# Kernel optimization log

Hardware: AMD Instinct MI355X
Metric: run time of the kernel (lower is better)

## Reference

```python
import jax, jax.numpy as jnp
from jax import lax
import numpy as np

B, T, D_IN = 4, 1024, 8
D_MODEL, N_LAYERS, HORIZON, D_OUT = 512, 2, 24, 8
D_STATE, D_CONV, EXPAND = 64, 4, 2
D_INNER = EXPAND * D_MODEL
DT_RANK = -(-D_MODEL // 16)  # ceil(d_model/16) = 32
LN_EPS = 1e-5


def setup_inputs() -> dict:
    key = jax.random.key(0)
    ks = iter(jax.random.split(key, 24))
    rn = lambda shape, s: jax.random.normal(next(ks), shape, jnp.float32) * s
    A_log = jnp.tile(jnp.log(jnp.arange(1, D_STATE + 1, dtype=jnp.float32)), (N_LAYERS, D_INNER, 1))
    return {
        "x": rn((B, T, D_IN), 1.0),
        "W_in": rn((D_IN, D_MODEL), 0.3), "b_in": jnp.zeros((D_MODEL,), jnp.float32),
        "W_xz": rn((N_LAYERS, D_MODEL, 2 * D_INNER), 0.04),
        "conv_w": rn((N_LAYERS, D_INNER, D_CONV), 0.3), "conv_b": jnp.zeros((N_LAYERS, D_INNER), jnp.float32),
        "W_xproj": rn((N_LAYERS, D_INNER, DT_RANK + 2 * D_STATE), 0.03),
        "W_dt": rn((N_LAYERS, DT_RANK, D_INNER), 0.1), "b_dt": rn((N_LAYERS, D_INNER), 0.1) - 4.0,
        "A_log": A_log, "D_skip": jnp.ones((N_LAYERS, D_INNER), jnp.float32),
        "W_out": rn((N_LAYERS, D_INNER, D_MODEL), 0.03),
        "ln_g": jnp.ones((D_MODEL,), jnp.float32), "ln_b": jnp.zeros((D_MODEL,), jnp.float32),
        "W_h1": rn((D_MODEL, D_MODEL), 0.04), "b_h1": jnp.zeros((D_MODEL,), jnp.float32),
        "W_h2": rn((D_MODEL, HORIZON * D_OUT), 0.04), "b_h2": jnp.zeros((HORIZON * D_OUT,), jnp.float32),
    }


def mamba_block(h, Wxz, cw, cb, Wxp, Wdt, bdt, Alog, Dsk, Wout):
    # h: [B,T,d_model] -> [B,T,d_model]  (mamba-ssm Mamba block, no residual)
    xz = h @ Wxz                                   # [B,T,2*d_inner]
    xb, z = jnp.split(xz, 2, axis=-1)
    # depthwise causal conv over time
    xc = jnp.transpose(xb, (0, 2, 1))              # [B,d_inner,T]
    xc = lax.conv_general_dilated(xc, cw[:, None, :], (1,), [(D_CONV - 1, 0)],
                                  feature_group_count=D_INNER)
    xc = jax.nn.silu(xc + cb[None, :, None])
    xc = jnp.transpose(xc, (0, 2, 1))              # [B,T,d_inner]
    # input-dependent dt, B, C
    xdb = xc @ Wxp                                 # [B,T,dt_rank+2*d_state]
    dt_r = xdb[..., :DT_RANK]
    Bc = xdb[..., DT_RANK:DT_RANK + D_STATE]
    Cc = xdb[..., DT_RANK + D_STATE:]
    dt = jax.nn.softplus(dt_r @ Wdt + bdt)         # [B,T,d_inner]
    A = -jnp.exp(Alog)                             # [d_inner,d_state]

    def step(hst, ins):
        dt_t, B_t, C_t, x_t = ins                  # [B,d_inner],[B,N],[B,N],[B,d_inner]
        dA = jnp.exp(dt_t[..., None] * A)          # [B,d_inner,N]
        hst = dA * hst + dt_t[..., None] * B_t[:, None, :] * x_t[..., None]
        y = jnp.einsum('bdn,bn->bd', hst, C_t)
        return hst, y

    h0 = jnp.zeros((h.shape[0], D_INNER, D_STATE), h.dtype)
    xs = (jnp.transpose(dt, (1, 0, 2)), jnp.transpose(Bc, (1, 0, 2)),
          jnp.transpose(Cc, (1, 0, 2)), jnp.transpose(xc, (1, 0, 2)))
    _, ys = lax.scan(step, h0, xs)                 # ys: [T,B,d_inner]
    y = jnp.transpose(ys, (1, 0, 2)) + Dsk * xc
    y = y * jax.nn.silu(z)
    return y @ Wout


def reference(x, W_in, b_in, W_xz, conv_w, conv_b, W_xproj, W_dt, b_dt, A_log, D_skip,
              W_out, ln_g, ln_b, W_h1, b_h1, W_h2, b_h2):
    h = x @ W_in + b_in                            # [B,T,d_model]
    for i in range(N_LAYERS):
        h = mamba_block(h, W_xz[i], conv_w[i], conv_b[i], W_xproj[i], W_dt[i],
                        b_dt[i], A_log[i], D_skip[i], W_out[i])
    mu = jnp.mean(h, axis=-1, keepdims=True)
    var = jnp.mean(jnp.square(h - mu), axis=-1, keepdims=True)
    h = (h - mu) * lax.rsqrt(var + LN_EPS) * ln_g + ln_b
    last = h[:, -1, :]                             # [B,d_model]
    hid = jax.nn.gelu(last @ W_h1 + b_h1, approximate=False)
    yhat = hid @ W_h2 + b_h2                       # [B,horizon*d_out]
    return yhat.reshape(x.shape[0], HORIZON, D_OUT)
```

## Files before the change

### kernel.cpp

```cpp
#include <hip/hip_runtime.h>
#include <hip/hip_bf16.h>

static constexpr int kB      = 4;
static constexpr int kT      = 1024;
static constexpr int kDIN    = 8;
static constexpr int kDMODEL = 512;
static constexpr int kNLAYER = 2;
static constexpr int kHOR    = 24;
static constexpr int kDOUT   = 8;
static constexpr int kDSTATE = 64;
static constexpr int kDINNER = 1024;
static constexpr int kDTRANK = 32;
static constexpr int kXPROJ  = 160;
static constexpr int kXPAD   = 256;
static constexpr int kBT     = kB * kT;

typedef __bf16 bf16x8 __attribute__((ext_vector_type(8)));
typedef float  f32x4  __attribute__((ext_vector_type(4)));

__device__ __forceinline__ float silu_f(float x)     { return x / (1.f + __expf(-x)); }
__device__ __forceinline__ float softplus_f(float x) { return (x > 20.f) ? x : log1pf(__expf(x)); }
__device__ __forceinline__ float gelu_f(float x)     { return 0.5f * x * (1.f + erff(x * 0.70710678118654752f)); }

__device__ __forceinline__ void gld_lds16(const void* g, void* l) {
    __builtin_amdgcn_global_load_lds(
        (const __attribute__((address_space(1))) unsigned int*)g,
        (__attribute__((address_space(3))) unsigned int*)l, 16, 0, 0);
}

__global__ __launch_bounds__(256) void wtrans_kernel(
    const float* __restrict__ in, int K, int N, int in_lstride,
    __hip_bfloat16* __restrict__ out, int Kpad, int out_lstride)
{
    __shared__ float tile[32][33];
    const int tid = threadIdx.x;
    const int n0 = blockIdx.x * 32;
    const int k0 = blockIdx.y * 32;
    const float* inl = in + (size_t)blockIdx.z * in_lstride;
    __hip_bfloat16* outl = out + (size_t)blockIdx.z * out_lstride;

#pragma unroll
    for (int p = 0; p < 4; ++p) {
        int idx = p * 256 + tid;
        int ki = idx >> 5, ni = idx & 31;
        float v = 0.f;
        if (k0 + ki < K && n0 + ni < N) v = inl[(size_t)(k0 + ki) * N + n0 + ni];
        tile[ki][ni] = v;
    }
    __syncthreads();
#pragma unroll
    for (int p = 0; p < 4; ++p) {
        int idx = p * 256 + tid;
        int ni = idx >> 5, ki = idx & 31;
        outl[(size_t)(n0 + ni) * Kpad + k0 + ki] = __float2bfloat16(tile[ki][ni]);
    }
}

template<int MODE>
__global__ __launch_bounds__(256) void mfma_gemm_bt(
    const __hip_bfloat16* __restrict__ A, int lda,
    const __hip_bfloat16* __restrict__ BT, int ldb,
    const float* __restrict__ bias,
    float* __restrict__ C, int ldc,
    void* __restrict__ C2,
    int K)
{
    __shared__ __align__(16) __hip_bfloat16 sA[128][64];
    __shared__ __align__(16) __hip_bfloat16 sB[128][64];

    const int tid  = threadIdx.x;
    const int lane = tid & 63;
    const int w    = tid >> 6;
    const int wm   = w >> 1, wn = w & 1;
    const int m0   = blockIdx.y * 128;
    const int n0   = blockIdx.x * 128;

    f32x4 acc[4][4] = {};

    const int lrow = lane & 15;
    const int lk   = (lane >> 4) << 3;

    const int grow = tid >> 3;
    const int gcol = (tid & 7) * 8;
    char* ldsA = (char*)&sA[0][0] + w * 1024;
    char* ldsB = (char*)&sB[0][0] + w * 1024;

    for (int k0 = 0; k0 < K; k0 += 64) {
        __syncthreads();
#pragma unroll
        for (int p = 0; p < 4; ++p) {
            gld_lds16(A  + (size_t)(m0 + grow + p * 32) * lda + k0 + gcol, ldsA + p * 4096);
            gld_lds16(BT + (size_t)(n0 + grow + p * 32) * ldb + k0 + gcol, ldsB + p * 4096);
        }
        __syncthreads();
#pragma unroll
        for (int ks = 0; ks < 2; ++ks) {
            bf16x8 af[4], bfr[4];
#pragma unroll
            for (int i = 0; i < 4; ++i) {
                af[i]  = *reinterpret_cast<const bf16x8*>(&sA[wm * 64 + i * 16 + lrow][ks * 32 + lk]);
                bfr[i] = *reinterpret_cast<const bf16x8*>(&sB[wn * 64 + i * 16 + lrow][ks * 32 + lk]);
            }
#pragma unroll
            for (int i = 0; i < 4; ++i)
#pragma unroll
                for (int j = 0; j < 4; ++j)
                    acc[i][j] = __builtin_amdgcn_mfma_f32_16x16x32_bf16(af[i], bfr[j], acc[i][j], 0, 0, 0);
        }
    }

    const int crow = (lane >> 4) * 4;
    const int ccol = lane & 15;
#pragma unroll
    for (int i = 0; i < 4; ++i) {
#pragma unroll
        for (int j = 0; j < 4; ++j) {
#pragma unroll
            for (int r = 0; r < 4; ++r) {
                int row = m0 + wm * 64 + i * 16 + crow + r;
                int col = n0 + wn * 64 + j * 16 + ccol;
                float v = acc[i][j][r];
                if (MODE == 0) {
                    if (col < kDINNER)
                        C[(size_t)row * ldc + col] = v;
                    else
                        ((__hip_bfloat16*)C2)[(size_t)row * ldc + (col - kDINNER)] =
                            __float2bfloat16(silu_f(v));
                } else if (MODE == 1) {
                    C[(size_t)row * ldc + col] = v;
                    ((__hip_bfloat16*)C2)[(size_t)row * ldc + col] = __float2bfloat16(v);
                } else {
                    C[(size_t)row * ldc + col] = softplus_f(v + bias[col]);
                }
            }
        }
    }
}

__global__ __launch_bounds__(256) void in_proj_kernel(
    const float* __restrict__ x, const float* __restrict__ W,
    const float* __restrict__ b,
    float* __restrict__ h, __hip_bfloat16* __restrict__ hb)
{
    int idx = blockIdx.x * 256 + threadIdx.x;
    int m = idx >> 9, n = idx & 511;
    float acc = b[n];
    const float* xr = x + m * kDIN;
#pragma unroll
    for (int k = 0; k < kDIN; ++k)
        acc = fmaf(xr[k], W[k * kDMODEL + n], acc);
    h[idx]  = acc;
    hb[idx] = __float2bfloat16(acc);
}

__global__ __launch_bounds__(256) void conv_silu_kernel(
    const float* __restrict__ xb,
    const float* __restrict__ cw, const float* __restrict__ cb,
    __hip_bfloat16* __restrict__ xc)
{
    int idx = blockIdx.x * 256 + threadIdx.x;
    int d   = idx & (kDINNER - 1);
    int bt  = idx >> 10;
    int t   = bt & (kT - 1);

    float4 wv = *reinterpret_cast<const float4*>(cw + d * 4);
    float acc = cb[d];
    const float* base = xb + (size_t)bt * kDINNER + d;
    if (t >= 3) {
        acc = fmaf(base[-3 * kDINNER], wv.x, acc);
        acc = fmaf(base[-2 * kDINNER], wv.y, acc);
        acc = fmaf(base[-1 * kDINNER], wv.z, acc);
        acc = fmaf(base[0],            wv.w, acc);
    } else {
        if (t >= 2) acc = fmaf(base[-2 * kDINNER], wv.y, acc);
        if (t >= 1) acc = fmaf(base[-1 * kDINNER], wv.z, acc);
        acc = fmaf(base[0], wv.w, acc);
    }
    xc[idx] = __float2bfloat16(silu_f(acc));
}

__global__ __launch_bounds__(256) void scan_kernel(
    const float* __restrict__ dt,
    const float* __restrict__ xdb,
    const __hip_bfloat16* __restrict__ xc,
    const __hip_bfloat16* __restrict__ zs,
    const float* __restrict__ Alog,
    const float* __restrict__ Dsk,
    __hip_bfloat16* __restrict__ yg)
{
    __shared__ float sBC[32][128];
    __shared__ float sDX[32][4][2];
    __shared__ float sY [32][4];

    const int tid  = threadIdx.x;
    const int lane = tid & 63;
    const int w    = tid >> 6;
    const int bb   = blockIdx.x;
    const int b    = bb >> 8;
    const int d0   = (bb & 255) * 4;
    const int d    = d0 + w;

    const float a   = -__expf(Alog[d * kDSTATE + lane]);
    const float dsk = Dsk[d];
    float s = 0.f;
    const size_t rowbase = (size_t)b * kT;

    const int hr = (tid & 127) >> 2, hj = tid & 3, hs = tid >> 7;

    for (int c = 0; c < kT / 32; ++c) {
        const int t0 = c * 32;
        __syncthreads();
#pragma unroll
        for (int p = 0; p < 4; ++p) {
            int idx = tid + p * 256;
            int r = idx >> 5, c4 = idx & 31;
            *reinterpret_cast<float4*>(&sBC[r][c4 * 4]) =
                *reinterpret_cast<const float4*>(xdb + (rowbase + t0 + r) * kXPAD + kDTRANK + c4 * 4);
        }
        {
            size_t g = (rowbase + t0 + hr) * kDINNER + d0 + hj;
            if (hs == 0) sDX[hr][hj][0] = dt[g];
            else         sDX[hr][hj][1] = __bfloat162float(xc[g]);
        }
        __syncthreads();

        float yv[32];
#pragma unroll
        for (int i = 0; i < 32; ++i) {
            float Bv  = sBC[i][lane];
            float Cv  = sBC[i][64 + lane];
            float dtv = sDX[i][w][0];
            float xv  = sDX[i][w][1];
            float dA  = __expf(dtv * a);
            s = fmaf(dA, s, (dtv * xv) * Bv);
            yv[i] = s * Cv;
        }

#pragma unroll
        for (int j = 0; j < 5; ++j) {
            const int S = 1 << j;
            const bool sel = (lane & S) != 0;
#pragma unroll
            for (int m = 0; m < (32 >> (j + 1)); ++m) {
                float av = yv[2 * m], bv2 = yv[2 * m + 1];
                float cv = sel ? bv2 : av;
                float dv = sel ? av : bv2;
                yv[m] = cv + __shfl_xor(dv, S, 64);
            }
        }
        float y = yv[0];
        y += __shfl_xor(y, 32, 64);

        if (lane < 32) sY[lane][w] = fmaf(dsk, sDX[lane][w][1], y);
        __syncthreads();
        if (tid < 128) {
            int r = tid >> 2, j = tid & 3;
            size_t g = (rowbase + t0 + r) * kDINNER + d0 + j;
            yg[g] = __float2bfloat16(sY[r][j] * __bfloat162float(zs[g]));
        }
    }
}

template<int N, int KK, int ACT>
__global__ __launch_bounds__(256) void head_gemm(
    const float* __restrict__ A,
    const float* __restrict__ B,
    const float* __restrict__ bias,
    float* __restrict__ C)
{
    const int n = blockIdx.x * 64 + (threadIdx.x & 63);
    const int b = threadIdx.x >> 6;
    const float* a  = A + b * KK;
    const float* bp = B + n;
    float acc = 0.f;
#pragma unroll 16
    for (int k = 0; k < KK; ++k)
        acc = fmaf(a[k], bp[(size_t)k * N], acc);
    float v = acc + bias[n];
    if (ACT == 3) v = gelu_f(v);
    C[(size_t)b * N + n] = v;
}

__global__ __launch_bounds__(256) void ln_last_kernel(
    const float* __restrict__ h,
    const float* __restrict__ g, const float* __restrict__ be,
    float* __restrict__ out)
{
    __shared__ float sbuf[8];
    int b = blockIdx.x, tid = threadIdx.x;
    const float* row = h + (size_t)(b * kT + (kT - 1)) * kDMODEL;

    float v0 = row[tid], v1 = row[tid + 256];
    float s = v0 + v1;
    float q = v0 * v0 + v1 * v1;
#pragma unroll
    for (int m = 32; m >= 1; m >>= 1) {
        s += __shfl_xor(s, m, 64);
        q += __shfl_xor(q, m, 64);
    }
    int wid = tid >> 6;
    if ((tid & 63) == 0) { sbuf[wid] = s; sbuf[4 + wid] = q; }
    __syncthreads();
    if (tid == 0) {
        float S = 0.f, Q = 0.f;
        for (int i = 0; i < 4; ++i) { S += sbuf[i]; Q += sbuf[4 + i]; }
        sbuf[0] = S; sbuf[4] = Q;
    }
    __syncthreads();
    float mean = sbuf[0] * (1.f / kDMODEL);
    float var  = sbuf[4] * (1.f / kDMODEL) - mean * mean;
    float inv  = rsqrtf(var + 1e-5f);
    out[b * kDMODEL + tid]       = (v0 - mean) * inv * g[tid]       + be[tid];
    out[b * kDMODEL + tid + 256] = (v1 - mean) * inv * g[tid + 256] + be[tid + 256];
}

extern "C" void kernel_launch(void* const* d_in, const int* in_sizes, int n_in,
                              void* d_out, int out_size, void* d_ws, size_t ws_size,
                              hipStream_t stream)
{
    const float* x      = (const float*)d_in[0];
    const float* W_in   = (const float*)d_in[1];
    const float* b_in   = (const float*)d_in[2];
    const float* W_xz   = (const float*)d_in[3];
    const float* conv_w = (const float*)d_in[4];
    const float* conv_b = (const float*)d_in[5];
    const float* W_xp   = (const float*)d_in[6];
    const float* W_dt   = (const float*)d_in[7];
    const float* b_dt   = (const float*)d_in[8];
    const float* A_log  = (const float*)d_in[9];
    const float* D_skip = (const float*)d_in[10];
    const float* W_out  = (const float*)d_in[11];
    const float* ln_g   = (const float*)d_in[12];
    const float* ln_b   = (const float*)d_in[13];
    const float* W_h1   = (const float*)d_in[14];
    const float* b_h1   = (const float*)d_in[15];
    const float* W_h2   = (const float*)d_in[16];
    const float* b_h2   = (const float*)d_in[17];
    float* out = (float*)d_out;

    char* p = (char*)d_ws;
    auto alloc = [&](size_t bytes) { char* q = p; p += (bytes + 255) & ~(size_t)255; return q; };
    float*          h       = (float*)         alloc((size_t)kBT * kDMODEL * 4);
    __hip_bfloat16* h_bf    = (__hip_bfloat16*)alloc((size_t)kBT * kDMODEL * 2);
    float*          xb      = (float*)         alloc((size_t)kBT * kDINNER * 4);
    __hip_bfloat16* z_bf    = (__hip_bfloat16*)alloc((size_t)kBT * kDINNER * 2);
    __hip_bfloat16* xc_bf   = (__hip_bfloat16*)alloc((size_t)kBT * kDINNER * 2);
    float*          xdb     = (float*)         alloc((size_t)kBT * kXPAD * 4);
    __hip_bfloat16* xdb_bf  = (__hip_bfloat16*)alloc((size_t)kBT * kXPAD * 2);
    __hip_bfloat16* ys_bf   = (__hip_bfloat16*)alloc((size_t)kBT * kDINNER * 2);
    __hip_bfloat16* wxz_bt  = (__hip_bfloat16*)alloc((size_t)2 * 2048 * 512 * 2);
    __hip_bfloat16* wxp_bt  = (__hip_bfloat16*)alloc((size_t)2 * 256 * 1024 * 2);
    __hip_bfloat16* wdt_bt  = (__hip_bfloat16*)alloc((size_t)2 * 1024 * 64 * 2);
    __hip_bfloat16* wout_bt = (__hip_bfloat16*)alloc((size_t)2 * 512 * 1024 * 2);
    float*          lnb     = (float*)         alloc(kB * kDMODEL * 4);
    float*          hid     = (float*)         alloc(kB * kDMODEL * 4);
    float*          dtb     = xb;

    wtrans_kernel<<<dim3(64, 16, 2), 256, 0, stream>>>(W_xz, 512,  2048, 512 * 2048, wxz_bt,  512,  2048 * 512);
    wtrans_kernel<<<dim3(8,  32, 2), 256, 0, stream>>>(W_xp, 1024, 160,  1024 * 160, wxp_bt,  1024, 256 * 1024);
    wtrans_kernel<<<dim3(32, 2,  2), 256, 0, stream>>>(W_dt, 32,   1024, 32 * 1024,  wdt_bt,  64,   1024 * 64);
    wtrans_kernel<<<dim3(16, 32, 2), 256, 0, stream>>>(W_out, 1024, 512, 1024 * 512, wout_bt, 1024, 512 * 1024);

    in_proj_kernel<<<(kBT * kDMODEL) / 256, 256, 0, stream>>>(x, W_in, b_in, h, h_bf);

    for (int l = 0; l < kNLAYER; ++l) {
        const float* cw_l  = conv_w + (size_t)l * kDINNER * 4;
        const float* cb_l  = conv_b + (size_t)l * kDINNER;
        const float* bdt_l = b_dt   + (size_t)l * kDINNER;
        const float* Al_l  = A_log  + (size_t)l * kDINNER * kDSTATE;
        const float* Dsk_l = D_skip + (size_t)l * kDINNER;
        const __hip_bfloat16* wxz_l  = wxz_bt  + (size_t)l * 2048 * 512;
        const __hip_bfloat16* wxp_l  = wxp_bt  + (size_t)l * 256 * 1024;
        const __hip_bfloat16* wdt_l  = wdt_bt  + (size_t)l * 1024 * 64;
        const __hip_bfloat16* wout_l = wout_bt + (size_t)l * 512 * 1024;

        mfma_gemm_bt<0><<<dim3(16, 32), 256, 0, stream>>>(
            h_bf, kDMODEL, wxz_l, 512, nullptr, xb, kDINNER, z_bf, kDMODEL);
        conv_silu_kernel<<<(kBT * kDINNER) / 256, 256, 0, stream>>>(xb, cw_l, cb_l, xc_bf);
        mfma_gemm_bt<1><<<dim3(2, 32), 256, 0, stream>>>(
            xc_bf, kDINNER, wxp_l, 1024, nullptr, xdb, kXPAD, xdb_bf, kDINNER);
        mfma_gemm_bt<2><<<dim3(8, 32), 256, 0, stream>>>(
            xdb_bf, kXPAD, wdt_l, 64, bdt_l, dtb, kDINNER, nullptr, 64);
        scan_kernel<<<kB * kDINNER / 4, 256, 0, stream>>>(
            dtb, xdb, xc_bf, z_bf, Al_l, Dsk_l, ys_bf);
        mfma_gemm_bt<1><<<dim3(4, 32), 256, 0, stream>>>(
            ys_bf, kDINNER, wout_l, 1024, nullptr, h, kDMODEL, h_bf, kDINNER);
    }

    ln_last_kernel<<<kB, 256, 0, stream>>>(h, ln_g, ln_b, lnb);
    head_gemm<kDMODEL, kDMODEL, 3><<<kDMODEL / 64, 256, 0, stream>>>(lnb, W_h1, b_h1, hid);
    head_gemm<kHOR * kDOUT, kDMODEL, 0><<<(kHOR * kDOUT) / 64, 256, 0, stream>>>(hid, W_h2, b_h2, out);
}
```

Baseline: 544.6 us.

## Double-buffer scan staging with async LDS loads, DPP reductions, bf16 xb

After: 528.5 us. 3.0% less time.

```diff
diff --git a/kernel.cpp b/kernel.cpp
--- a/kernel.cpp
+++ b/kernel.cpp
@@ -28,6 +28,15 @@
         (__attribute__((address_space(3))) unsigned int*)l, 16, 0, 0);
 }
 
+__device__ __forceinline__ float readlane_f(float v, int l) {
+    return __int_as_float(__builtin_amdgcn_readlane(__float_as_int(v), l));
+}
+template<int CTRL>
+__device__ __forceinline__ float dpp_mov(float v) {
+    return __int_as_float(__builtin_amdgcn_update_dpp(
+        0, __float_as_int(v), CTRL, 0xf, 0xf, false));
+}
+
 __global__ __launch_bounds__(256) void wtrans_kernel(
     const float* __restrict__ in, int K, int N, int in_lstride,
     __hip_bfloat16* __restrict__ out, int Kpad, int out_lstride)
@@ -120,17 +129,17 @@
                 int row = m0 + wm * 64 + i * 16 + crow + r;
                 int col = n0 + wn * 64 + j * 16 + ccol;
                 float v = acc[i][j][r];
-                if (MODE == 0) {
+                if (MODE == 1) {
+                    C[(size_t)row * ldc + col] = v;
+                    ((__hip_bfloat16*)C2)[(size_t)row * ldc + col] = __float2bfloat16(v);
+                } else if (MODE == 2) {
+                    C[(size_t)row * ldc + col] = softplus_f(v + bias[col]);
+                } else {
                     if (col < kDINNER)
-                        C[(size_t)row * ldc + col] = v;
+                        ((__hip_bfloat16*)C)[(size_t)row * ldc + col] = __float2bfloat16(v);
                     else
                         ((__hip_bfloat16*)C2)[(size_t)row * ldc + (col - kDINNER)] =
                             __float2bfloat16(silu_f(v));
-                } else if (MODE == 1) {
-                    C[(size_t)row * ldc + col] = v;
-                    ((__hip_bfloat16*)C2)[(size_t)row * ldc + col] = __float2bfloat16(v);
-                } else {
-                    C[(size_t)row * ldc + col] = softplus_f(v + bias[col]);
                 }
             }
         }
@@ -154,7 +163,7 @@
 }
 
 __global__ __launch_bounds__(256) void conv_silu_kernel(
-    const float* __restrict__ xb,
+    const __hip_bfloat16* __restrict__ xb,
     const float* __restrict__ cw, const float* __restrict__ cb,
     __hip_bfloat16* __restrict__ xc)
 {
@@ -165,21 +174,21 @@
 
     float4 wv = *reinterpret_cast<const float4*>(cw + d * 4);
     float acc = cb[d];
-    const float* base = xb + (size_t)bt * kDINNER + d;
+    const __hip_bfloat16* base = xb + (size_t)bt * kDINNER + d;
     if (t >= 3) {
-        acc = fmaf(base[-3 * kDINNER], wv.x, acc);
-        acc = fmaf(base[-2 * kDINNER], wv.y, acc);
-        acc = fmaf(base[-1 * kDINNER], wv.z, acc);
-        acc = fmaf(base[0],            wv.w, acc);
+        acc = fmaf(__bfloat162float(base[-3 * kDINNER]), wv.x, acc);
+        acc = fmaf(__bfloat162float(base[-2 * kDINNER]), wv.y, acc);
+        acc = fmaf(__bfloat162float(base[-1 * kDINNER]), wv.z, acc);
+        acc = fmaf(__bfloat162float(base[0]),            wv.w, acc);
     } else {
-        if (t >= 2) acc = fmaf(base[-2 * kDINNER], wv.y, acc);
-        if (t >= 1) acc = fmaf(base[-1 * kDINNER], wv.z, acc);
-        acc = fmaf(base[0], wv.w, acc);
+        if (t >= 2) acc = fmaf(__bfloat162float(base[-2 * kDINNER]), wv.y, acc);
+        if (t >= 1) acc = fmaf(__bfloat162float(base[-1 * kDINNER]), wv.z, acc);
+        acc = fmaf(__bfloat162float(base[0]), wv.w, acc);
     }
     xc[idx] = __float2bfloat16(silu_f(acc));
 }
 
-__global__ __launch_bounds__(256) void scan_kernel(
+__global__ __launch_bounds__(256, 4) void scan_kernel(
     const float* __restrict__ dt,
     const float* __restrict__ xdb,
     const __hip_bfloat16* __restrict__ xc,
@@ -188,75 +197,101 @@
     const float* __restrict__ Dsk,
     __hip_bfloat16* __restrict__ yg)
 {
-    __shared__ float sBC[32][128];
-    __shared__ float sDX[32][4][2];
-    __shared__ float sY [32][4];
+    __shared__ __align__(16) float sBC[2][32][128];
+    __shared__ float sY[2][32][4];
 
     const int tid  = threadIdx.x;
     const int lane = tid & 63;
     const int w    = tid >> 6;
-    const int bb   = blockIdx.x;
-    const int b    = bb >> 8;
-    const int d0   = (bb & 255) * 4;
-    const int d    = d0 + w;
-
-    const float a   = -__expf(Alog[d * kDSTATE + lane]);
+    const int bb = blockIdx.x;
+    const int b  = (bb & 7) >> 1;
+    const int d0 = ((bb >> 3) + (bb & 1) * 128) * 4;
+    const int d  = d0 + w;
+
+    const float a2  = -__expf(Alog[d * kDSTATE + lane]) * 1.44269504f;
     const float dsk = Dsk[d];
+    const size_t rowbase = (size_t)b * kT;
     float s = 0.f;
-    const size_t rowbase = (size_t)b * kT;
-
-    const int hr = (tid & 127) >> 2, hj = tid & 3, hs = tid >> 7;
-
-    for (int c = 0; c < kT / 32; ++c) {
-        const int t0 = c * 32;
-        __syncthreads();
-#pragma unroll
-        for (int p = 0; p < 4; ++p) {
-            int idx = tid + p * 256;
-            int r = idx >> 5, c4 = idx & 31;
-            *reinterpret_cast<float4*>(&sBC[r][c4 * 4]) =
-                *reinterpret_cast<const float4*>(xdb + (rowbase + t0 + r) * kXPAD + kDTRANK + c4 * 4);
-        }
-        {
-            size_t g = (rowbase + t0 + hr) * kDINNER + d0 + hj;
-            if (hs == 0) sDX[hr][hj][0] = dt[g];
-            else         sDX[hr][hj][1] = __bfloat162float(xc[g]);
-        }
-        __syncthreads();
-
-        float yv[32];
-#pragma unroll
-        for (int i = 0; i < 32; ++i) {
-            float Bv  = sBC[i][lane];
-            float Cv  = sBC[i][64 + lane];
-            float dtv = sDX[i][w][0];
-            float xv  = sDX[i][w][1];
-            float dA  = __expf(dtv * a);
-            s = fmaf(dA, s, (dtv * xv) * Bv);
-            yv[i] = s * Cv;
-        }
-
-#pragma unroll
-        for (int j = 0; j < 5; ++j) {
-            const int S = 1 << j;
-            const bool sel = (lane & S) != 0;
-#pragma unroll
-            for (int m = 0; m < (32 >> (j + 1)); ++m) {
-                float av = yv[2 * m], bv2 = yv[2 * m + 1];
-                float cv = sel ? bv2 : av;
-                float dv = sel ? av : bv2;
-                yv[m] = cv + __shfl_xor(dv, S, 64);
-            }
-        }
-        float y = yv[0];
-        y += __shfl_xor(y, 32, 64);
-
-        if (lane < 32) sY[lane][w] = fmaf(dsk, sDX[lane][w][1], y);
-        __syncthreads();
-        if (tid < 128) {
-            int r = tid >> 2, j = tid & 3;
-            size_t g = (rowbase + t0 + r) * kDINNER + d0 + j;
-            yg[g] = __float2bfloat16(sY[r][j] * __bfloat162float(zs[g]));
+
+    auto stage = [&](int c, int buf) {
+        const float* src = xdb + (rowbase + c * 32 + w * 8 + (lane >> 5)) * kXPAD
+                               + kDTRANK + (lane & 31) * 4;
+#pragma unroll
+        for (int p = 0; p < 4; ++p)
+            gld_lds16(src + p * 2 * kXPAD, &sBC[buf][w * 8 + p * 2][0]);
+    };
+    auto loadpair = [&](int pr, float& odt, float& oxc, float& odtx) {
+        size_t row = rowbase + pr * 64 + lane;
+        odt  = dt[row * kDINNER + d];
+        oxc  = __bfloat162float(xc[row * kDINNER + d]);
+        odtx = odt * oxc;
+    };
+
+    float vdt, vxc, vdtx;
+    stage(0, 0);
+    loadpair(0, vdt, vxc, vdtx);
+    __syncthreads();
+
+    for (int pr = 0; pr < kT / 64; ++pr) {
+#pragma unroll
+        for (int half = 0; half < 2; ++half) {
+            const int c   = pr * 2 + half;
+            const int buf = half;
+            if (c + 1 < kT / 32) stage(c + 1, buf ^ 1);
+            float ndt, nxc, ndtx;
+            const bool ld = (half == 1) && (pr + 1 < kT / 64);
+            if (ld) loadpair(pr + 1, ndt, nxc, ndtx);
+
+            float yv[32];
+#pragma unroll
+            for (int i = 0; i < 32; ++i) {
+                float Bv   = sBC[buf][i][lane];
+                float Cv   = sBC[buf][i][64 + lane];
+                float sdt  = readlane_f(vdt,  half * 32 + i);
+                float sdtx = readlane_f(vdtx, half * 32 + i);
+                float dA   = exp2f(sdt * a2);
+                s = fmaf(dA, s, sdtx * Bv);
+                yv[i] = s * Cv;
+            }
+
+#pragma unroll
+            for (int m = 0; m < 16; ++m) {
+                float av = yv[2 * m], bv = yv[2 * m + 1];
+                float cv = (lane & 1) ? bv : av;
+                float dv = (lane & 1) ? av : bv;
+                yv[m] = cv + dpp_mov<0xB1>(dv);
+            }
+#pragma unroll
+            for (int m = 0; m < 8; ++m) {
+                float av = yv[2 * m], bv = yv[2 * m + 1];
+                float cv = (lane & 2) ? bv : av;
+                float dv = (lane & 2) ? av : bv;
+                yv[m] = cv + dpp_mov<0x4E>(dv);
+            }
+#pragma unroll
+            for (int j = 2; j < 5; ++j) {
+                const int S = 1 << j;
+#pragma unroll
+                for (int m = 0; m < (32 >> (j + 1)); ++m) {
+                    float av = yv[2 * m], bv = yv[2 * m + 1];
+                    float cv = (lane & S) ? bv : av;
+                    float dv = (lane & S) ? av : bv;
+                    yv[m] = cv + __shfl_xor(dv, S, 64);
+                }
+            }
+            float y = yv[0];
+            y += __shfl_xor(y, 32, 64);
+
+            if ((lane & 32) == half * 32)
+                sY[buf][lane & 31][w] = fmaf(dsk, vxc, y);
+            __syncthreads();
+
+            if (tid < 128) {
+                int r = tid >> 2, j2 = tid & 3;
+                size_t g = (rowbase + c * 32 + r) * kDINNER + d0 + j2;
+                yg[g] = __float2bfloat16(sY[buf][r][j2] * __bfloat162float(zs[g]));
+            }
+            if (ld) { vdt = ndt; vxc = nxc; vdtx = ndtx; }
         }
     }
 }
@@ -342,11 +377,12 @@
     auto alloc = [&](size_t bytes) { char* q = p; p += (bytes + 255) & ~(size_t)255; return q; };
     float*          h       = (float*)         alloc((size_t)kBT * kDMODEL * 4);
     __hip_bfloat16* h_bf    = (__hip_bfloat16*)alloc((size_t)kBT * kDMODEL * 2);
-    float*          xb      = (float*)         alloc((size_t)kBT * kDINNER * 4);
+    __hip_bfloat16* xb_bf   = (__hip_bfloat16*)alloc((size_t)kBT * kDINNER * 2);
     __hip_bfloat16* z_bf    = (__hip_bfloat16*)alloc((size_t)kBT * kDINNER * 2);
     __hip_bfloat16* xc_bf   = (__hip_bfloat16*)alloc((size_t)kBT * kDINNER * 2);
     float*          xdb     = (float*)         alloc((size_t)kBT * kXPAD * 4);
     __hip_bfloat16* xdb_bf  = (__hip_bfloat16*)alloc((size_t)kBT * kXPAD * 2);
+    float*          dtb     = (float*)         alloc((size_t)kBT * kDINNER * 4);
     __hip_bfloat16* ys_bf   = (__hip_bfloat16*)alloc((size_t)kBT * kDINNER * 2);
     __hip_bfloat16* wxz_bt  = (__hip_bfloat16*)alloc((size_t)2 * 2048 * 512 * 2);
     __hip_bfloat16* wxp_bt  = (__hip_bfloat16*)alloc((size_t)2 * 256 * 1024 * 2);
@@ -354,7 +390,6 @@
     __hip_bfloat16* wout_bt = (__hip_bfloat16*)alloc((size_t)2 * 512 * 1024 * 2);
     float*          lnb     = (float*)         alloc(kB * kDMODEL * 4);
     float*          hid     = (float*)         alloc(kB * kDMODEL * 4);
-    float*          dtb     = xb;
 
     wtrans_kernel<<<dim3(64, 16, 2), 256, 0, stream>>>(W_xz, 512,  2048, 512 * 2048, wxz_bt,  512,  2048 * 512);
     wtrans_kernel<<<dim3(8,  32, 2), 256, 0, stream>>>(W_xp, 1024, 160,  1024 * 160, wxp_bt,  1024, 256 * 1024);
@@ -374,9 +409,9 @@
         const __hip_bfloat16* wdt_l  = wdt_bt  + (size_t)l * 1024 * 64;
         const __hip_bfloat16* wout_l = wout_bt + (size_t)l * 512 * 1024;
 
-        mfma_gemm_bt<0><<<dim3(16, 32), 256, 0, stream>>>(
-            h_bf, kDMODEL, wxz_l, 512, nullptr, xb, kDINNER, z_bf, kDMODEL);
-        conv_silu_kernel<<<(kBT * kDINNER) / 256, 256, 0, stream>>>(xb, cw_l, cb_l, xc_bf);
+        mfma_gemm_bt<4><<<dim3(16, 32), 256, 0, stream>>>(
+            h_bf, kDMODEL, wxz_l, 512, nullptr, (float*)xb_bf, kDINNER, z_bf, kDMODEL);
+        conv_silu_kernel<<<(kBT * kDINNER) / 256, 256, 0, stream>>>(xb_bf, cw_l, cb_l, xc_bf);
         mfma_gemm_bt<1><<<dim3(2, 32), 256, 0, stream>>>(
             xc_bf, kDINNER, wxp_l, 1024, nullptr, xdb, kXPAD, xdb_bf, kDINNER);
         mfma_gemm_bt<2><<<dim3(8, 32), 256, 0, stream>>>(
```
